# Kernel tuning notes

Measured on AMD Instinct MI355X. Metric: run time of the kernel, lower is better.

Reference implementation:

```python
import jax, jax.numpy as jnp
import numpy as np

N0, N1, N2 = 1200000, 120000, 12000  # nodes per hop (outermost -> seeds)
E0, E1 = 1200000, 120000
IN_C, HID_C, OUT_C = 256, 256, 64


def setup_inputs() -> dict:
    key = jax.random.key(0)
    ks = jax.random.split(key, 10)
    s_in, s_hid = 1.0 / np.sqrt(IN_C), 1.0 / np.sqrt(HID_C)
    return {
        "x": jax.random.normal(ks[0], (N0, IN_C), dtype=jnp.float32),
        "src0": jax.random.randint(ks[1], (E0,), 0, N0, dtype=jnp.int64),
        "dst0": jax.random.randint(ks[2], (E0,), 0, N1, dtype=jnp.int64),
        "src1": jax.random.randint(ks[3], (E1,), 0, N1, dtype=jnp.int64),
        "dst1": jax.random.randint(ks[4], (E1,), 0, N2, dtype=jnp.int64),
        "Wl0": jax.random.normal(ks[5], (HID_C, IN_C), dtype=jnp.float32) * s_in,
        "b0": jnp.zeros((HID_C,), dtype=jnp.float32),
        "Wr0": jax.random.normal(ks[6], (HID_C, IN_C), dtype=jnp.float32) * s_in,
        "Wl1": jax.random.normal(ks[7], (OUT_C, HID_C), dtype=jnp.float32) * s_hid,
        "b1": jnp.zeros((OUT_C,), dtype=jnp.float32),
        "Wr1": jax.random.normal(ks[8], (OUT_C, HID_C), dtype=jnp.float32) * s_hid,
    }


def _sage_conv(x_src, x_tgt, src, dst, Wl, b, Wr, n_tgt):
    # gather neighbor (source) features, mean-scatter onto targets
    msg = x_src[src]                                          # [E, C]
    agg = jax.ops.segment_sum(msg, dst, num_segments=n_tgt)   # [n_tgt, C]
    cnt = jax.ops.segment_sum(jnp.ones((dst.shape[0],), x_src.dtype), dst,
                              num_segments=n_tgt)
    agg = agg / jnp.maximum(cnt, 1.0)[:, None]
    return agg @ Wl.T + b + x_tgt @ Wr.T


def reference(x, src0, dst0, src1, dst1, Wl0, b0, Wr0, Wl1, b1, Wr1):
    # layer 0 (eval mode: dropout is identity)
    h = _sage_conv(x, x[:N1], src0, dst0, Wl0, b0, Wr0, N1)
    h = jax.nn.relu(h)
    # layer 1
    out = _sage_conv(h, h[:N2], src1, dst1, Wl1, b1, Wr1, N2)
    return jax.nn.log_softmax(out, axis=-1)
```

## Files before the change

kernel.cpp:

```cpp
#include <hip/hip_runtime.h>

#define N0c 1200000
#define N1c 120000
#define N2c 12000
#define E0c 1200000
#define E1c 120000
#define NB0 118
#define NB1 12

typedef short short8 __attribute__((ext_vector_type(8)));
typedef float f32x4 __attribute__((ext_vector_type(4)));
typedef unsigned short u16;

__device__ __forceinline__ u16 f2bf(float f) {
    union { float f; unsigned u; } v; v.f = f;
    unsigned r = v.u + 0x7FFFu + ((v.u >> 16) & 1u);
    return (u16)(r >> 16);
}
__device__ __forceinline__ float bf2f(u16 h) {
    union { unsigned u; float f; } v; v.u = ((unsigned)h) << 16;
    return v.f;
}

__global__ void k_hist(const int* __restrict__ dst0, const int* __restrict__ dst1,
                       int* __restrict__ c0, int* __restrict__ c1) {
    int i = blockIdx.x * 256 + threadIdx.x;
    int part = blockIdx.x & 7;
    if (i < E0c) atomicAdd(&c0[part * N1c + dst0[i]], 1);
    else if (i < E0c + E1c) atomicAdd(&c1[part * N2c + dst1[i - E0c]], 1);
}

__global__ void k_scanA(const int* __restrict__ c0, const int* __restrict__ c1,
                        int* __restrict__ partials) {
    __shared__ int sh[256];
    int hop = blockIdx.x >= NB0;
    int blk = hop ? blockIdx.x - NB0 : blockIdx.x;
    const int* c = hop ? c1 : c0;
    int n = hop ? N2c : N1c;
    int d0 = blk * 1024 + threadIdx.x * 4;
    int tsum = 0;
#pragma unroll
    for (int j = 0; j < 4; ++j) {
        int d = d0 + j;
        if (d < n)
#pragma unroll
            for (int k = 0; k < 8; ++k) tsum += c[k * n + d];
    }
    sh[threadIdx.x] = tsum;
    __syncthreads();
    for (int ofs = 128; ofs > 0; ofs >>= 1) {
        if (threadIdx.x < ofs) sh[threadIdx.x] += sh[threadIdx.x + ofs];
        __syncthreads();
    }
    if (threadIdx.x == 0) partials[blockIdx.x] = sh[0];
}

__global__ void k_scanB(int* __restrict__ partials, int* __restrict__ rs0,
                        int* __restrict__ rs1) {
    __shared__ int sh[256];
    int tid = threadIdx.x;
    int v0 = tid < NB0 ? partials[tid] : 0;
    sh[tid] = v0; __syncthreads();
    for (int ofs = 1; ofs < 256; ofs <<= 1) {
        int t = tid >= ofs ? sh[tid - ofs] : 0;
        __syncthreads();
        sh[tid] += t;
        __syncthreads();
    }
    if (tid < NB0) partials[tid] = sh[tid] - v0;
    __syncthreads();
    int v1 = tid < NB1 ? partials[NB0 + tid] : 0;
    sh[tid] = v1; __syncthreads();
    for (int ofs = 1; ofs < 256; ofs <<= 1) {
        int t = tid >= ofs ? sh[tid - ofs] : 0;
        __syncthreads();
        sh[tid] += t;
        __syncthreads();
    }
    if (tid < NB1) partials[NB0 + tid] = sh[tid] - v1;
    if (tid == 0) { rs0[N1c] = E0c; rs1[N2c] = E1c; }
}

__global__ void k_scanC(const int* __restrict__ c0, const int* __restrict__ c1,
                        const int* __restrict__ partials, int* __restrict__ rs0,
                        int* __restrict__ rs1, int* __restrict__ bs0,
                        int* __restrict__ bs1) {
    __shared__ int sh[256];
    int hop = blockIdx.x >= NB0;
    int blk = hop ? blockIdx.x - NB0 : blockIdx.x;
    const int* c = hop ? c1 : c0;
    int* rs = hop ? rs1 : rs0;
    int* bs = hop ? bs1 : bs0;
    int n = hop ? N2c : N1c;
    int tid = threadIdx.x;
    int d0 = blk * 1024 + tid * 4;
    int cv[4][8];
    int tsum = 0;
#pragma unroll
    for (int j = 0; j < 4; ++j)
#pragma unroll
        for (int k = 0; k < 8; ++k) {
            int d = d0 + j;
            int v = (d < n) ? c[k * n + d] : 0;
            cv[j][k] = v; tsum += v;
        }
    sh[tid] = tsum; __syncthreads();
    for (int ofs = 1; ofs < 256; ofs <<= 1) {
        int t = tid >= ofs ? sh[tid - ofs] : 0;
        __syncthreads();
        sh[tid] += t;
        __syncthreads();
    }
    int run = partials[blockIdx.x] + sh[tid] - tsum;
#pragma unroll
    for (int j = 0; j < 4; ++j) {
        int d = d0 + j;
        if (d < n) {
            rs[d] = run;
#pragma unroll
            for (int k = 0; k < 8; ++k) { bs[k * n + d] = run; run += cv[j][k]; }
        }
    }
}

__global__ void k_scat(const int* __restrict__ src0, const int* __restrict__ dst0,
                       const int* __restrict__ src1, const int* __restrict__ dst1,
                       int* __restrict__ c0, int* __restrict__ c1,
                       const int* __restrict__ bs0, const int* __restrict__ bs1,
                       int* __restrict__ eidx0, int* __restrict__ eidx1) {
    int i = blockIdx.x * 256 + threadIdx.x;
    int part = blockIdx.x & 7;
    if (i < E0c) {
        int d = dst0[i];
        int off = atomicSub(&c0[part * N1c + d], 1) - 1;
        eidx0[bs0[part * N1c + d] + off] = src0[i];
    } else if (i < E0c + E1c) {
        int j = i - E0c;
        int d = dst1[j];
        int off = atomicSub(&c1[part * N2c + d], 1) - 1;
        eidx1[bs1[part * N2c + d] + off] = src1[j];
    }
}

__global__ void k_wcat2(u16* __restrict__ Bt0, const float* __restrict__ Wl0,
                        const float* __restrict__ Wr0, u16* __restrict__ Bt1,
                        const float* __restrict__ Wl1, const float* __restrict__ Wr1) {
    int i = blockIdx.x * blockDim.x + threadIdx.x;
    if (i < 256 * 512) {
        int c = i >> 9, k = i & 511;
        float v = (k < 256) ? Wl0[c * 256 + k] : Wr0[c * 256 + (k - 256)];
        Bt0[i] = f2bf(v);
    } else if (i < 256 * 512 + 128 * 512) {
        int j = i - 256 * 512;
        int c = j >> 9, k = j & 511;
        float v = 0.f;
        if (c < 64) v = (k < 256) ? Wl1[c * 256 + k] : Wr1[c * 256 + (k - 256)];
        Bt1[j] = f2bf(v);
    }
}

__global__ void k_agg0(const float* __restrict__ x, const int* __restrict__ eidx,
                       const int* __restrict__ rs, u16* __restrict__ A, int ntgt) {
    int w = (int)((blockIdx.x * blockDim.x + threadIdx.x) >> 6);
    int lane = threadIdx.x & 63;
    if (w >= ntgt) return;
    int s = rs[w], e = rs[w + 1];
    float a0 = 0.f, a1 = 0.f, a2 = 0.f, a3 = 0.f;
    int i = s;
    for (; i + 8 <= e; i += 8) {
        float4 v[8];
#pragma unroll
        for (int u = 0; u < 8; ++u) {
            long idx = eidx[i + u];
            v[u] = ((const float4*)(x + idx * 256))[lane];
        }
#pragma unroll
        for (int u = 0; u < 8; ++u) {
            a0 += v[u].x; a1 += v[u].y; a2 += v[u].z; a3 += v[u].w;
        }
    }
    for (; i + 2 <= e; i += 2) {
        long i0 = eidx[i], i1 = eidx[i + 1];
        float4 v0 = ((const float4*)(x + i0 * 256))[lane];
        float4 v1 = ((const float4*)(x + i1 * 256))[lane];
        a0 += v0.x + v1.x; a1 += v0.y + v1.y; a2 += v0.z + v1.z; a3 += v0.w + v1.w;
    }
    if (i < e) {
        long idx = eidx[i];
        float4 v = ((const float4*)(x + idx * 256))[lane];
        a0 += v.x; a1 += v.y; a2 += v.z; a3 += v.w;
    }
    int c = e - s; if (c < 1) c = 1;
    float sc = 1.f / (float)c;
    ushort4 o;
    o.x = f2bf(a0 * sc); o.y = f2bf(a1 * sc); o.z = f2bf(a2 * sc); o.w = f2bf(a3 * sc);
    *(ushort4*)(A + (long)w * 512 + lane * 4) = o;
    float4 sv = ((const float4*)(x + (long)w * 256))[lane];
    ushort4 so;
    so.x = f2bf(sv.x); so.y = f2bf(sv.y); so.z = f2bf(sv.z); so.w = f2bf(sv.w);
    *(ushort4*)(A + (long)w * 512 + 256 + lane * 4) = so;
}

__global__ void k_agg1(const u16* __restrict__ hsrc, const int* __restrict__ eidx,
                       const int* __restrict__ rs, u16* __restrict__ A, int ntgt) {
    int w = (int)((blockIdx.x * blockDim.x + threadIdx.x) >> 6);
    int lane = threadIdx.x & 63;
    if (w >= ntgt) return;
    int s = rs[w], e = rs[w + 1];
    float a0 = 0.f, a1 = 0.f, a2 = 0.f, a3 = 0.f;
    int i = s;
    for (; i + 4 <= e; i += 4) {
        long i0 = eidx[i], i1 = eidx[i + 1], i2 = eidx[i + 2], i3 = eidx[i + 3];
        ushort4 v0 = ((const ushort4*)(hsrc + i0 * 256))[lane];
        ushort4 v1 = ((const ushort4*)(hsrc + i1 * 256))[lane];
        ushort4 v2 = ((const ushort4*)(hsrc + i2 * 256))[lane];
        ushort4 v3 = ((const ushort4*)(hsrc + i3 * 256))[lane];
        a0 += (bf2f(v0.x) + bf2f(v1.x)) + (bf2f(v2.x) + bf2f(v3.x));
        a1 += (bf2f(v0.y) + bf2f(v1.y)) + (bf2f(v2.y) + bf2f(v3.y));
        a2 += (bf2f(v0.z) + bf2f(v1.z)) + (bf2f(v2.z) + bf2f(v3.z));
        a3 += (bf2f(v0.w) + bf2f(v1.w)) + (bf2f(v2.w) + bf2f(v3.w));
    }
    for (; i < e; ++i) {
        long idx = eidx[i];
        ushort4 v = ((const ushort4*)(hsrc + idx * 256))[lane];
        a0 += bf2f(v.x); a1 += bf2f(v.y); a2 += bf2f(v.z); a3 += bf2f(v.w);
    }
    int c = e - s; if (c < 1) c = 1;
    float sc = 1.f / (float)c;
    ushort4 o;
    o.x = f2bf(a0 * sc); o.y = f2bf(a1 * sc); o.z = f2bf(a2 * sc); o.w = f2bf(a3 * sc);
    *(ushort4*)(A + (long)w * 512 + lane * 4) = o;
    ushort4 sv = ((const ushort4*)(hsrc + (long)w * 256))[lane];
    *(ushort4*)(A + (long)w * 512 + 256 + lane * 4) = sv;
}

#define BM 128
#define BK 32
#define LDK 40

template <int WN, bool RELU_BF16>
__global__ __launch_bounds__(128 * WN)
void k_gemm(const u16* __restrict__ A, const u16* __restrict__ Bt,
            const float* __restrict__ bias, void* __restrict__ outp,
            int M, int Ncols, int ldo) {
    constexpr int BN_ = WN * 64;
    constexpr int APT = 4 / WN;
    constexpr int WSH = (WN == 4) ? 2 : 1;
    __shared__ u16 As[BM * LDK];
    __shared__ u16 Bs[BN_ * LDK];
    const int tid = threadIdx.x;
    const int lane = tid & 63, wid = tid >> 6;
    const int wm = wid >> WSH, wn = wid & (WN - 1);
    const long m0 = (long)blockIdx.x * BM;
    const int n0 = blockIdx.y * BN_;
    const int sar = tid / WN, sac = (tid % WN) * (APT * 8);
    const int sbr = tid >> 1, sbc = (tid & 1) * 16;

    f32x4 acc[4][4];
#pragma unroll
    for (int i = 0; i < 4; ++i)
#pragma unroll
        for (int j = 0; j < 4; ++j) acc[i][j] = (f32x4){0.f, 0.f, 0.f, 0.f};

    int4 ra[APT]; int4 rb[2];

    auto load_tile = [&](int ks) {
        int k0 = ks * BK;
        const int4* p = (const int4*)(A + (m0 + sar) * 512 + k0 + sac);
#pragma unroll
        for (int t = 0; t < APT; ++t) ra[t] = p[t];
        const int4* q = (const int4*)(Bt + (long)(n0 + sbr) * 512 + k0 + sbc);
        rb[0] = q[0]; rb[1] = q[1];
    };

    auto write_tile = [&]() {
        int4* da = (int4*)(As + sar * LDK + sac);
#pragma unroll
        for (int t = 0; t < APT; ++t) da[t] = ra[t];
        int4* db = (int4*)(Bs + sbr * LDK + sbc);
        db[0] = rb[0]; db[1] = rb[1];
    };

    load_tile(0);
    const int NK = 512 / BK;
    for (int ks = 0; ks < NK; ++ks) {
        __syncthreads();
        write_tile();
        __syncthreads();
        if (ks + 1 < NK) load_tile(ks + 1);
        short8 af[4], bv[4];
        const int rr = lane & 15, gg = lane >> 4;
#pragma unroll
        for (int f = 0; f < 4; ++f) {
            af[f] = *(const short8*)(As + (wm * 64 + f * 16 + rr) * LDK + gg * 8);
            bv[f] = *(const short8*)(Bs + (wn * 64 + f * 16 + rr) * LDK + gg * 8);
        }
#pragma unroll
        for (int i = 0; i < 4; ++i)
#pragma unroll
            for (int j = 0; j < 4; ++j)
                acc[i][j] =
                    __builtin_amdgcn_mfma_f32_16x16x32_bf16(af[i], bv[j], acc[i][j], 0, 0, 0);
    }

#pragma unroll
    for (int j = 0; j < 4; ++j) {
        int col = n0 + wn * 64 + j * 16 + (lane & 15);
        if (col >= Ncols) continue;
        float bvl = bias[col];
#pragma unroll
        for (int i = 0; i < 4; ++i) {
            long row = m0 + wm * 64 + i * 16 + (lane >> 4) * 4;
#pragma unroll
            for (int q = 0; q < 4; ++q) {
                long r = row + q;
                if (r < M) {
                    float v = acc[i][j][q] + bvl;
                    if (RELU_BF16) {
                        v = v > 0.f ? v : 0.f;
                        ((u16*)outp)[r * (long)ldo + col] = f2bf(v);
                    } else {
                        ((float*)outp)[r * (long)ldo + col] = v;
                    }
                }
            }
        }
    }
}

__global__ void k_lsm(const float* __restrict__ lg, float* __restrict__ out, int nrows) {
    int w = (int)((blockIdx.x * blockDim.x + threadIdx.x) >> 6);
    int lane = threadIdx.x & 63;
    if (w >= nrows) return;
    float v = lg[(long)w * 64 + lane];
    float m = v;
    for (int d = 32; d > 0; d >>= 1) m = fmaxf(m, __shfl_xor(m, d, 64));
    float ex = __expf(v - m);
    float s = ex;
    for (int d = 32; d > 0; d >>= 1) s += __shfl_xor(s, d, 64);
    out[(long)w * 64 + lane] = v - m - __logf(s);
}

extern "C" void kernel_launch(void* const* d_in, const int* in_sizes, int n_in,
                              void* d_out, int out_size, void* d_ws, size_t ws_size,
                              hipStream_t stream) {
    const float* x   = (const float*)d_in[0];
    const int* src0  = (const int*)d_in[1];
    const int* dst0  = (const int*)d_in[2];
    const int* src1  = (const int*)d_in[3];
    const int* dst1  = (const int*)d_in[4];
    const float* Wl0 = (const float*)d_in[5];
    const float* b0  = (const float*)d_in[6];
    const float* Wr0 = (const float*)d_in[7];
    const float* Wl1 = (const float*)d_in[8];
    const float* b1  = (const float*)d_in[9];
    const float* Wr1 = (const float*)d_in[10];

    char* base = (char*)d_ws;
    size_t off = 0;
    auto alloc = [&](size_t bytes) -> void* {
        off = (off + 255) & ~(size_t)255;
        void* p = base + off;
        off += bytes;
        return p;
    };
    const int N1pad = 120064, N2pad = 12032;
    int* c0       = (int*)alloc((size_t)8 * N1c * 4);
    int* c1       = (int*)alloc((size_t)8 * N2c * 4);
    int* bs0      = (int*)alloc((size_t)8 * N1c * 4);
    int* bs1      = (int*)alloc((size_t)8 * N2c * 4);
    int* rs0      = (int*)alloc((size_t)(N1c + 1) * 4);
    int* rs1      = (int*)alloc((size_t)(N2c + 1) * 4);
    int* partials = (int*)alloc((size_t)(NB0 + NB1) * 4);
    int* eidx0    = (int*)alloc((size_t)E0c * 4);
    int* eidx1    = (int*)alloc((size_t)E1c * 4);
    u16* A0       = (u16*)alloc((size_t)N1pad * 512 * 2);
    u16* hbuf     = (u16*)alloc((size_t)N1pad * 256 * 2);
    u16* A1       = (u16*)alloc((size_t)N2pad * 512 * 2);
    u16* Bt0      = (u16*)alloc((size_t)256 * 512 * 2);
    u16* Bt1      = (u16*)alloc((size_t)128 * 512 * 2);
    float* logits = (float*)alloc((size_t)N2pad * 64 * 4);

    hipMemsetAsync(c0, 0, (size_t)8 * (N1c + N2c) * 4, stream);

    const int Etot = E0c + E1c;
    k_hist<<<(Etot + 255) / 256, 256, 0, stream>>>(dst0, dst1, c0, c1);
    k_scanA<<<NB0 + NB1, 256, 0, stream>>>(c0, c1, partials);
    k_scanB<<<1, 256, 0, stream>>>(partials, rs0, rs1);
    k_scanC<<<NB0 + NB1, 256, 0, stream>>>(c0, c1, partials, rs0, rs1, bs0, bs1);
    k_scat<<<(Etot + 255) / 256, 256, 0, stream>>>(src0, dst0, src1, dst1,
                                                   c0, c1, bs0, bs1, eidx0, eidx1);

    k_wcat2<<<(256 * 512 + 128 * 512 + 255) / 256, 256, 0, stream>>>(Bt0, Wl0, Wr0,
                                                                     Bt1, Wl1, Wr1);

    k_agg0<<<(N1c + 3) / 4, 256, 0, stream>>>(x, eidx0, rs0, A0, N1c);
    dim3 g0(N1pad / BM, 1);
    k_gemm<4, true><<<g0, 512, 0, stream>>>(A0, Bt0, b0, hbuf, N1c, 256, 256);

    k_agg1<<<(N2c + 3) / 4, 256, 0, stream>>>(hbuf, eidx1, rs1, A1, N2c);
    dim3 g1(N2pad / BM, 1);
    k_gemm<2, false><<<g1, 256, 0, stream>>>(A1, Bt1, b1, logits, N2c, 64, 64);

    k_lsm<<<(N2c + 3) / 4, 256, 0, stream>>>(logits, (float*)d_out, N2c);
}
```

Before: 592.0 us.

## Fuse neighbor aggregation into GEMM via swizzled LDS A-tile, fold log-softmax

Each layer's mean aggregation now writes its bf16 concatenated [agg | self] row block straight into a 128KB XOR-swizzled shared-memory tile, and the block then runs the MFMA GEMM from that tile. This removes the global A0/A1 round trips and separate kernel launches. Layer 1 also computes log-softmax in the GEMM epilogue with 16-lane shuffles, which drops the logits buffer and the k_lsm kernel. In exchange, 128KB of LDS per block limits occupancy to about one block per CU, so the latency-bound gather phase gets less parallelism and cannot overlap with the GEMM.

```diff
diff --git a/kernel.cpp b/kernel.cpp
--- a/kernel.cpp
+++ b/kernel.cpp
@@ -150,150 +150,98 @@
         int c = i >> 9, k = i & 511;
         float v = (k < 256) ? Wl0[c * 256 + k] : Wr0[c * 256 + (k - 256)];
         Bt0[i] = f2bf(v);
-    } else if (i < 256 * 512 + 128 * 512) {
+    } else if (i < 256 * 512 + 64 * 512) {
         int j = i - 256 * 512;
         int c = j >> 9, k = j & 511;
-        float v = 0.f;
-        if (c < 64) v = (k < 256) ? Wl1[c * 256 + k] : Wr1[c * 256 + (k - 256)];
+        float v = (k < 256) ? Wl1[c * 256 + k] : Wr1[c * 256 + (k - 256)];
         Bt1[j] = f2bf(v);
     }
 }
 
-__global__ void k_agg0(const float* __restrict__ x, const int* __restrict__ eidx,
-                       const int* __restrict__ rs, u16* __restrict__ A, int ntgt) {
-    int w = (int)((blockIdx.x * blockDim.x + threadIdx.x) >> 6);
-    int lane = threadIdx.x & 63;
-    if (w >= ntgt) return;
-    int s = rs[w], e = rs[w + 1];
-    float a0 = 0.f, a1 = 0.f, a2 = 0.f, a3 = 0.f;
-    int i = s;
-    for (; i + 8 <= e; i += 8) {
-        float4 v[8];
-#pragma unroll
-        for (int u = 0; u < 8; ++u) {
-            long idx = eidx[i + u];
-            v[u] = ((const float4*)(x + idx * 256))[lane];
-        }
-#pragma unroll
-        for (int u = 0; u < 8; ++u) {
-            a0 += v[u].x; a1 += v[u].y; a2 += v[u].z; a3 += v[u].w;
-        }
-    }
-    for (; i + 2 <= e; i += 2) {
-        long i0 = eidx[i], i1 = eidx[i + 1];
-        float4 v0 = ((const float4*)(x + i0 * 256))[lane];
-        float4 v1 = ((const float4*)(x + i1 * 256))[lane];
-        a0 += v0.x + v1.x; a1 += v0.y + v1.y; a2 += v0.z + v1.z; a3 += v0.w + v1.w;
-    }
-    if (i < e) {
-        long idx = eidx[i];
-        float4 v = ((const float4*)(x + idx * 256))[lane];
-        a0 += v.x; a1 += v.y; a2 += v.z; a3 += v.w;
-    }
-    int c = e - s; if (c < 1) c = 1;
-    float sc = 1.f / (float)c;
-    ushort4 o;
-    o.x = f2bf(a0 * sc); o.y = f2bf(a1 * sc); o.z = f2bf(a2 * sc); o.w = f2bf(a3 * sc);
-    *(ushort4*)(A + (long)w * 512 + lane * 4) = o;
-    float4 sv = ((const float4*)(x + (long)w * 256))[lane];
-    ushort4 so;
-    so.x = f2bf(sv.x); so.y = f2bf(sv.y); so.z = f2bf(sv.z); so.w = f2bf(sv.w);
-    *(ushort4*)(A + (long)w * 512 + 256 + lane * 4) = so;
-}
-
-__global__ void k_agg1(const u16* __restrict__ hsrc, const int* __restrict__ eidx,
-                       const int* __restrict__ rs, u16* __restrict__ A, int ntgt) {
-    int w = (int)((blockIdx.x * blockDim.x + threadIdx.x) >> 6);
-    int lane = threadIdx.x & 63;
-    if (w >= ntgt) return;
-    int s = rs[w], e = rs[w + 1];
-    float a0 = 0.f, a1 = 0.f, a2 = 0.f, a3 = 0.f;
-    int i = s;
-    for (; i + 4 <= e; i += 4) {
-        long i0 = eidx[i], i1 = eidx[i + 1], i2 = eidx[i + 2], i3 = eidx[i + 3];
-        ushort4 v0 = ((const ushort4*)(hsrc + i0 * 256))[lane];
-        ushort4 v1 = ((const ushort4*)(hsrc + i1 * 256))[lane];
-        ushort4 v2 = ((const ushort4*)(hsrc + i2 * 256))[lane];
-        ushort4 v3 = ((const ushort4*)(hsrc + i3 * 256))[lane];
-        a0 += (bf2f(v0.x) + bf2f(v1.x)) + (bf2f(v2.x) + bf2f(v3.x));
-        a1 += (bf2f(v0.y) + bf2f(v1.y)) + (bf2f(v2.y) + bf2f(v3.y));
-        a2 += (bf2f(v0.z) + bf2f(v1.z)) + (bf2f(v2.z) + bf2f(v3.z));
-        a3 += (bf2f(v0.w) + bf2f(v1.w)) + (bf2f(v2.w) + bf2f(v3.w));
-    }
-    for (; i < e; ++i) {
-        long idx = eidx[i];
-        ushort4 v = ((const ushort4*)(hsrc + idx * 256))[lane];
-        a0 += bf2f(v.x); a1 += bf2f(v.y); a2 += bf2f(v.z); a3 += bf2f(v.w);
-    }
-    int c = e - s; if (c < 1) c = 1;
-    float sc = 1.f / (float)c;
-    ushort4 o;
-    o.x = f2bf(a0 * sc); o.y = f2bf(a1 * sc); o.z = f2bf(a2 * sc); o.w = f2bf(a3 * sc);
-    *(ushort4*)(A + (long)w * 512 + lane * 4) = o;
-    ushort4 sv = ((const ushort4*)(hsrc + (long)w * 256))[lane];
-    *(ushort4*)(A + (long)w * 512 + 256 + lane * 4) = sv;
-}
-
-#define BM 128
-#define BK 32
-#define LDK 40
-
-template <int WN, bool RELU_BF16>
-__global__ __launch_bounds__(128 * WN)
-void k_gemm(const u16* __restrict__ A, const u16* __restrict__ Bt,
-            const float* __restrict__ bias, void* __restrict__ outp,
-            int M, int Ncols, int ldo) {
-    constexpr int BN_ = WN * 64;
-    constexpr int APT = 4 / WN;
-    constexpr int WSH = (WN == 4) ? 2 : 1;
-    __shared__ u16 As[BM * LDK];
-    __shared__ u16 Bs[BN_ * LDK];
+__device__ __forceinline__ int aoff(int row, int byteInRow) {
+    return row * 1024 + (byteInRow ^ ((row & 7) << 4));
+}
+
+__global__ __launch_bounds__(512)
+void k_fused0(const float* __restrict__ x, const int* __restrict__ eidx,
+              const int* __restrict__ rs, const u16* __restrict__ Bt,
+              const float* __restrict__ bias, u16* __restrict__ outp) {
+    __shared__ u16 Asm[128 * 512];
+    __shared__ u16 Bsm[256 * 40];
     const int tid = threadIdx.x;
     const int lane = tid & 63, wid = tid >> 6;
-    const int wm = wid >> WSH, wn = wid & (WN - 1);
-    const long m0 = (long)blockIdx.x * BM;
-    const int n0 = blockIdx.y * BN_;
-    const int sar = tid / WN, sac = (tid % WN) * (APT * 8);
-    const int sbr = tid >> 1, sbc = (tid & 1) * 16;
-
+    const long m0 = (long)blockIdx.x * 128;
+
+    for (int t = 0; t < 16; ++t) {
+        int wl = wid * 16 + t;
+        long w = m0 + wl;
+        float a0 = 0.f, a1 = 0.f, a2 = 0.f, a3 = 0.f;
+        float s0 = 0.f, s1 = 0.f, s2 = 0.f, s3 = 0.f;
+        if (w < N1c) {
+            int s = rs[w], e = rs[w + 1];
+            int i = s;
+            for (; i + 8 <= e; i += 8) {
+                float4 v[8];
+#pragma unroll
+                for (int u = 0; u < 8; ++u)
+                    v[u] = ((const float4*)(x + (long)eidx[i + u] * 256))[lane];
+#pragma unroll
+                for (int u = 0; u < 8; ++u) {
+                    a0 += v[u].x; a1 += v[u].y; a2 += v[u].z; a3 += v[u].w;
+                }
+            }
+            for (; i + 2 <= e; i += 2) {
+                float4 v0 = ((const float4*)(x + (long)eidx[i] * 256))[lane];
+                float4 v1 = ((const float4*)(x + (long)eidx[i + 1] * 256))[lane];
+                a0 += v0.x + v1.x; a1 += v0.y + v1.y;
+                a2 += v0.z + v1.z; a3 += v0.w + v1.w;
+            }
+            if (i < e) {
+                float4 v = ((const float4*)(x + (long)eidx[i] * 256))[lane];
+                a0 += v.x; a1 += v.y; a2 += v.z; a3 += v.w;
+            }
+            int c = e - s; if (c < 1) c = 1;
+            float sc = 1.f / (float)c;
+            a0 *= sc; a1 *= sc; a2 *= sc; a3 *= sc;
+            float4 sv = ((const float4*)(x + w * 256))[lane];
+            s0 = sv.x; s1 = sv.y; s2 = sv.z; s3 = sv.w;
+        }
+        ushort4 oa; oa.x = f2bf(a0); oa.y = f2bf(a1); oa.z = f2bf(a2); oa.w = f2bf(a3);
+        *(ushort4*)((char*)Asm + aoff(wl, lane * 8)) = oa;
+        ushort4 os; os.x = f2bf(s0); os.y = f2bf(s1); os.z = f2bf(s2); os.w = f2bf(s3);
+        *(ushort4*)((char*)Asm + aoff(wl, 512 + lane * 8)) = os;
+    }
+
+    const int wm = wid >> 2, wn = wid & 3;
+    const int brow = tid >> 1, bcol = (tid & 1) * 16;
     f32x4 acc[4][4];
 #pragma unroll
     for (int i = 0; i < 4; ++i)
 #pragma unroll
         for (int j = 0; j < 4; ++j) acc[i][j] = (f32x4){0.f, 0.f, 0.f, 0.f};
-
-    int4 ra[APT]; int4 rb[2];
-
-    auto load_tile = [&](int ks) {
-        int k0 = ks * BK;
-        const int4* p = (const int4*)(A + (m0 + sar) * 512 + k0 + sac);
-#pragma unroll
-        for (int t = 0; t < APT; ++t) ra[t] = p[t];
-        const int4* q = (const int4*)(Bt + (long)(n0 + sbr) * 512 + k0 + sbc);
-        rb[0] = q[0]; rb[1] = q[1];
-    };
-
-    auto write_tile = [&]() {
-        int4* da = (int4*)(As + sar * LDK + sac);
-#pragma unroll
-        for (int t = 0; t < APT; ++t) da[t] = ra[t];
-        int4* db = (int4*)(Bs + sbr * LDK + sbc);
-        db[0] = rb[0]; db[1] = rb[1];
-    };
-
-    load_tile(0);
-    const int NK = 512 / BK;
-    for (int ks = 0; ks < NK; ++ks) {
-        __syncthreads();
-        write_tile();
-        __syncthreads();
-        if (ks + 1 < NK) load_tile(ks + 1);
+    int4 rb0, rb1;
+    {
+        const int4* q = (const int4*)(Bt + (long)brow * 512 + bcol);
+        rb0 = q[0]; rb1 = q[1];
+    }
+    __syncthreads();
+    const int rr = lane & 15, gg = lane >> 4;
+    for (int ks = 0; ks < 16; ++ks) {
+        {
+            int4* d = (int4*)(Bsm + brow * 40 + bcol);
+            d[0] = rb0; d[1] = rb1;
+        }
+        __syncthreads();
+        if (ks < 15) {
+            const int4* q = (const int4*)(Bt + (long)brow * 512 + (ks + 1) * 32 + bcol);
+            rb0 = q[0]; rb1 = q[1];
+        }
         short8 af[4], bv[4];
-        const int rr = lane & 15, gg = lane >> 4;
 #pragma unroll
         for (int f = 0; f < 4; ++f) {
-            af[f] = *(const short8*)(As + (wm * 64 + f * 16 + rr) * LDK + gg * 8);
-            bv[f] = *(const short8*)(Bs + (wn * 64 + f * 16 + rr) * LDK + gg * 8);
+            af[f] = *(const short8*)((char*)Asm +
+                                     aoff(wm * 64 + f * 16 + rr, ks * 64 + gg * 16));
+            bv[f] = *(const short8*)(Bsm + (wn * 64 + f * 16 + rr) * 40 + gg * 8);
         }
 #pragma unroll
         for (int i = 0; i < 4; ++i)
@@ -301,44 +249,135 @@
             for (int j = 0; j < 4; ++j)
                 acc[i][j] =
                     __builtin_amdgcn_mfma_f32_16x16x32_bf16(af[i], bv[j], acc[i][j], 0, 0, 0);
+        __syncthreads();
     }
 
 #pragma unroll
     for (int j = 0; j < 4; ++j) {
-        int col = n0 + wn * 64 + j * 16 + (lane & 15);
-        if (col >= Ncols) continue;
+        int col = wn * 64 + j * 16 + rr;
         float bvl = bias[col];
 #pragma unroll
         for (int i = 0; i < 4; ++i) {
-            long row = m0 + wm * 64 + i * 16 + (lane >> 4) * 4;
+            long row = m0 + wm * 64 + i * 16 + gg * 4;
 #pragma unroll
             for (int q = 0; q < 4; ++q) {
                 long r = row + q;
-                if (r < M) {
+                if (r < N1c) {
                     float v = acc[i][j][q] + bvl;
-                    if (RELU_BF16) {
-                        v = v > 0.f ? v : 0.f;
-                        ((u16*)outp)[r * (long)ldo + col] = f2bf(v);
-                    } else {
-                        ((float*)outp)[r * (long)ldo + col] = v;
-                    }
+                    v = v > 0.f ? v : 0.f;
+                    outp[r * 256 + col] = f2bf(v);
                 }
             }
         }
     }
 }
 
-__global__ void k_lsm(const float* __restrict__ lg, float* __restrict__ out, int nrows) {
-    int w = (int)((blockIdx.x * blockDim.x + threadIdx.x) >> 6);
-    int lane = threadIdx.x & 63;
-    if (w >= nrows) return;
-    float v = lg[(long)w * 64 + lane];
-    float m = v;
-    for (int d = 32; d > 0; d >>= 1) m = fmaxf(m, __shfl_xor(m, d, 64));
-    float ex = __expf(v - m);
-    float s = ex;
-    for (int d = 32; d > 0; d >>= 1) s += __shfl_xor(s, d, 64);
-    out[(long)w * 64 + lane] = v - m - __logf(s);
+__global__ __launch_bounds__(256)
+void k_fused1(const u16* __restrict__ hsrc, const int* __restrict__ eidx,
+              const int* __restrict__ rs, const u16* __restrict__ Bt,
+              const float* __restrict__ bias, float* __restrict__ outp) {
+    __shared__ u16 Asm[128 * 512];
+    __shared__ u16 Bsm[64 * 40];
+    const int tid = threadIdx.x;
+    const int lane = tid & 63, wid = tid >> 6;
+    const long m0 = (long)blockIdx.x * 128;
+
+    for (int t = 0; t < 32; ++t) {
+        int wl = wid * 32 + t;
+        long w = m0 + wl;
+        float a0 = 0.f, a1 = 0.f, a2 = 0.f, a3 = 0.f;
+        ushort4 sv; sv.x = 0; sv.y = 0; sv.z = 0; sv.w = 0;
+        if (w < N2c) {
+            int s = rs[w], e = rs[w + 1];
+            int i = s;
+            for (; i + 4 <= e; i += 4) {
+                ushort4 v0 = ((const ushort4*)(hsrc + (long)eidx[i] * 256))[lane];
+                ushort4 v1 = ((const ushort4*)(hsrc + (long)eidx[i + 1] * 256))[lane];
+                ushort4 v2 = ((const ushort4*)(hsrc + (long)eidx[i + 2] * 256))[lane];
+                ushort4 v3 = ((const ushort4*)(hsrc + (long)eidx[i + 3] * 256))[lane];
+                a0 += (bf2f(v0.x) + bf2f(v1.x)) + (bf2f(v2.x) + bf2f(v3.x));
+                a1 += (bf2f(v0.y) + bf2f(v1.y)) + (bf2f(v2.y) + bf2f(v3.y));
+                a2 += (bf2f(v0.z) + bf2f(v1.z)) + (bf2f(v2.z) + bf2f(v3.z));
+                a3 += (bf2f(v0.w) + bf2f(v1.w)) + (bf2f(v2.w) + bf2f(v3.w));
+            }
+            for (; i < e; ++i) {
+                ushort4 v = ((const ushort4*)(hsrc + (long)eidx[i] * 256))[lane];
+                a0 += bf2f(v.x); a1 += bf2f(v.y); a2 += bf2f(v.z); a3 += bf2f(v.w);
+            }
+            int c = e - s; if (c < 1) c = 1;
+            float sc = 1.f / (float)c;
+            a0 *= sc; a1 *= sc; a2 *= sc; a3 *= sc;
+            sv = ((const ushort4*)(hsrc + w * 256))[lane];
+        }
+        ushort4 oa; oa.x = f2bf(a0); oa.y = f2bf(a1); oa.z = f2bf(a2); oa.w = f2bf(a3);
+        *(ushort4*)((char*)Asm + aoff(wl, lane * 8)) = oa;
+        *(ushort4*)((char*)Asm + aoff(wl, 512 + lane * 8)) = sv;
+    }
+
+    const int wm = wid;
+    const bool bact = tid < 128;
+    const int brow = tid >> 1, bcol = (tid & 1) * 16;
+    f32x4 acc[2][4];
+#pragma unroll
+    for (int i = 0; i < 2; ++i)
+#pragma unroll
+        for (int j = 0; j < 4; ++j) acc[i][j] = (f32x4){0.f, 0.f, 0.f, 0.f};
+    int4 rb0, rb1;
+    if (bact) {
+        const int4* q = (const int4*)(Bt + (long)brow * 512 + bcol);
+        rb0 = q[0]; rb1 = q[1];
+    }
+    __syncthreads();
+    const int rr = lane & 15, gg = lane >> 4;
+    for (int ks = 0; ks < 16; ++ks) {
+        if (bact) {
+            int4* d = (int4*)(Bsm + brow * 40 + bcol);
+            d[0] = rb0; d[1] = rb1;
+        }
+        __syncthreads();
+        if (bact && ks < 15) {
+            const int4* q = (const int4*)(Bt + (long)brow * 512 + (ks + 1) * 32 + bcol);
+            rb0 = q[0]; rb1 = q[1];
+        }
+        short8 af[2], bv[4];
+#pragma unroll
+        for (int f = 0; f < 2; ++f)
+            af[f] = *(const short8*)((char*)Asm +
+                                     aoff(wm * 32 + f * 16 + rr, ks * 64 + gg * 16));
+#pragma unroll
+        for (int j = 0; j < 4; ++j)
+            bv[j] = *(const short8*)(Bsm + (j * 16 + rr) * 40 + gg * 8);
+#pragma unroll
+        for (int i = 0; i < 2; ++i)
+#pragma unroll
+            for (int j = 0; j < 4; ++j)
+                acc[i][j] =
+                    __builtin_amdgcn_mfma_f32_16x16x32_bf16(af[i], bv[j], acc[i][j], 0, 0, 0);
+        __syncthreads();
+    }
+
+#pragma unroll
+    for (int i = 0; i < 2; ++i) {
+#pragma unroll
+        for (int q = 0; q < 4; ++q) {
+            long r = m0 + wm * 32 + i * 16 + gg * 4 + q;
+            float v[4];
+#pragma unroll
+            for (int j = 0; j < 4; ++j) v[j] = acc[i][j][q] + bias[j * 16 + rr];
+            float mx = fmaxf(fmaxf(v[0], v[1]), fmaxf(v[2], v[3]));
+#pragma unroll
+            for (int msk = 1; msk < 16; msk <<= 1) mx = fmaxf(mx, __shfl_xor(mx, msk, 16));
+            float se = __expf(v[0] - mx) + __expf(v[1] - mx) +
+                       __expf(v[2] - mx) + __expf(v[3] - mx);
+#pragma unroll
+            for (int msk = 1; msk < 16; msk <<= 1) se += __shfl_xor(se, msk, 16);
+            float ln = __logf(se);
+            if (r < N2c) {
+#pragma unroll
+                for (int j = 0; j < 4; ++j) outp[r * 64 + j * 16 + rr] = v[j] - mx - ln;
+            }
+        }
+    }
 }
 
 extern "C" void kernel_launch(void* const* d_in, const int* in_sizes, int n_in,
@@ -364,7 +403,6 @@
         off += bytes;
         return p;
     };
-    const int N1pad = 120064, N2pad = 12032;
     int* c0       = (int*)alloc((size_t)8 * N1c * 4);
     int* c1       = (int*)alloc((size_t)8 * N2c * 4);
     int* bs0      = (int*)alloc((size_t)8 * N1c * 4);
@@ -374,12 +412,9 @@
     int* partials = (int*)alloc((size_t)(NB0 + NB1) * 4);
     int* eidx0    = (int*)alloc((size_t)E0c * 4);
     int* eidx1    = (int*)alloc((size_t)E1c * 4);
-    u16* A0       = (u16*)alloc((size_t)N1pad * 512 * 2);
-    u16* hbuf     = (u16*)alloc((size_t)N1pad * 256 * 2);
-    u16* A1       = (u16*)alloc((size_t)N2pad * 512 * 2);
+    u16* hbuf     = (u16*)alloc((size_t)N1c * 256 * 2);
     u16* Bt0      = (u16*)alloc((size_t)256 * 512 * 2);
-    u16* Bt1      = (u16*)alloc((size_t)128 * 512 * 2);
-    float* logits = (float*)alloc((size_t)N2pad * 64 * 4);
+    u16* Bt1      = (u16*)alloc((size_t)64 * 512 * 2);
 
     hipMemsetAsync(c0, 0, (size_t)8 * (N1c + N2c) * 4, stream);
 
@@ -391,16 +426,11 @@
     k_scat<<<(Etot + 255) / 256, 256, 0, stream>>>(src0, dst0, src1, dst1,
                                                    c0, c1, bs0, bs1, eidx0, eidx1);
 
-    k_wcat2<<<(256 * 512 + 128 * 512 + 255) / 256, 256, 0, stream>>>(Bt0, Wl0, Wr0,
-                                                                     Bt1, Wl1, Wr1);
-
-    k_agg0<<<(N1c + 3) / 4, 256, 0, stream>>>(x, eidx0, rs0, A0, N1c);
-    dim3 g0(N1pad / BM, 1);
-    k_gemm<4, true><<<g0, 512, 0, stream>>>(A0, Bt0, b0, hbuf, N1c, 256, 256);
-
-    k_agg1<<<(N2c + 3) / 4, 256, 0, stream>>>(hbuf, eidx1, rs1, A1, N2c);
-    dim3 g1(N2pad / BM, 1);
-    k_gemm<2, false><<<g1, 256, 0, stream>>>(A1, Bt1, b1, logits, N2c, 64, 64);
-
-    k_lsm<<<(N2c + 3) / 4, 256, 0, stream>>>(logits, (float*)d_out, N2c);
-}
+    k_wcat2<<<(256 * 512 + 64 * 512 + 255) / 256, 256, 0, stream>>>(Bt0, Wl0, Wr0,
+                                                                    Bt1, Wl1, Wr1);
+
+    k_fused0<<<(N1c + 127) / 128, 512, 0, stream>>>(x, eidx0, rs0, Bt0, b0, hbuf);
+
+    k_fused1<<<(N2c + 127) / 128, 256, 0, stream>>>(hbuf, eidx1, rs1, Bt1, b1,
+                                                    (float*)d_out);
+}
```

After: 652.8 us. 10.3% more time.

## Pre-tile A0 and Bt0 into padded k-slabs and add an async-LDS-load layer-0 GEMM

Applied to the files above, without the earlier changes.

The layer-0 activation matrix and weights are now stored as k-tiled slabs of 32 bf16 values padded to 40 per row, so each 128-row tile is one contiguous chunk. A new dedicated GEMM kernel copies those chunks straight into LDS with global_load_lds, double-buffered, and runs 16x16x32 bf16 MFMAs with a fused bias and ReLU epilogue. The aim is cheaper, bank-conflict-free tile staging and overlap of loads with compute. The cost is a scattered write pattern in the aggregation kernel and an epilogue that writes scalar, poorly coalesced bf16 values.

```diff
diff --git a/kernel.cpp b/kernel.cpp
--- a/kernel.cpp
+++ b/kernel.cpp
@@ -1,4 +1,5 @@
 #include <hip/hip_runtime.h>
+#include <stdint.h>
 
 #define N0c 1200000
 #define N1c 120000
@@ -7,6 +8,10 @@
 #define E1c 120000
 #define NB0 118
 #define NB1 12
+#define N1pad 120064
+#define N2pad 12032
+#define ROWB 80
+#define ROWU 40
 
 typedef short short8 __attribute__((ext_vector_type(8)));
 typedef float f32x4 __attribute__((ext_vector_type(4)));
@@ -20,6 +25,12 @@
 __device__ __forceinline__ float bf2f(u16 h) {
     union { unsigned u; float f; } v; v.u = ((unsigned)h) << 16;
     return v.f;
+}
+
+__device__ __forceinline__ void gload16(const char* g, char* l) {
+    __builtin_amdgcn_global_load_lds(
+        (const __attribute__((address_space(1))) void*)g,
+        (__attribute__((address_space(3))) void*)l, 16, 0, 0);
 }
 
 __global__ void k_hist(const int* __restrict__ dst0, const int* __restrict__ dst1,
@@ -149,7 +160,7 @@
     if (i < 256 * 512) {
         int c = i >> 9, k = i & 511;
         float v = (k < 256) ? Wl0[c * 256 + k] : Wr0[c * 256 + (k - 256)];
-        Bt0[i] = f2bf(v);
+        Bt0[((size_t)(k >> 5) * 256 + c) * ROWU + (k & 31)] = f2bf(v);
     } else if (i < 256 * 512 + 128 * 512) {
         int j = i - 256 * 512;
         int c = j >> 9, k = j & 511;
@@ -170,35 +181,33 @@
     for (; i + 8 <= e; i += 8) {
         float4 v[8];
 #pragma unroll
-        for (int u = 0; u < 8; ++u) {
-            long idx = eidx[i + u];
-            v[u] = ((const float4*)(x + idx * 256))[lane];
-        }
+        for (int u = 0; u < 8; ++u)
+            v[u] = ((const float4*)(x + (long)eidx[i + u] * 256))[lane];
 #pragma unroll
         for (int u = 0; u < 8; ++u) {
             a0 += v[u].x; a1 += v[u].y; a2 += v[u].z; a3 += v[u].w;
         }
     }
     for (; i + 2 <= e; i += 2) {
-        long i0 = eidx[i], i1 = eidx[i + 1];
-        float4 v0 = ((const float4*)(x + i0 * 256))[lane];
-        float4 v1 = ((const float4*)(x + i1 * 256))[lane];
+        float4 v0 = ((const float4*)(x + (long)eidx[i] * 256))[lane];
+        float4 v1 = ((const float4*)(x + (long)eidx[i + 1] * 256))[lane];
         a0 += v0.x + v1.x; a1 += v0.y + v1.y; a2 += v0.z + v1.z; a3 += v0.w + v1.w;
     }
     if (i < e) {
-        long idx = eidx[i];
-        float4 v = ((const float4*)(x + idx * 256))[lane];
+        float4 v = ((const float4*)(x + (long)eidx[i] * 256))[lane];
         a0 += v.x; a1 += v.y; a2 += v.z; a3 += v.w;
     }
     int c = e - s; if (c < 1) c = 1;
     float sc = 1.f / (float)c;
-    ushort4 o;
-    o.x = f2bf(a0 * sc); o.y = f2bf(a1 * sc); o.z = f2bf(a2 * sc); o.w = f2bf(a3 * sc);
-    *(ushort4*)(A + (long)w * 512 + lane * 4) = o;
+    int kt = lane >> 3;
+    int cu = (lane & 7) * 4;
+    ushort4 oa;
+    oa.x = f2bf(a0 * sc); oa.y = f2bf(a1 * sc); oa.z = f2bf(a2 * sc); oa.w = f2bf(a3 * sc);
+    *(ushort4*)(A + ((size_t)kt * N1pad + w) * ROWU + cu) = oa;
     float4 sv = ((const float4*)(x + (long)w * 256))[lane];
-    ushort4 so;
-    so.x = f2bf(sv.x); so.y = f2bf(sv.y); so.z = f2bf(sv.z); so.w = f2bf(sv.w);
-    *(ushort4*)(A + (long)w * 512 + 256 + lane * 4) = so;
+    ushort4 os;
+    os.x = f2bf(sv.x); os.y = f2bf(sv.y); os.z = f2bf(sv.z); os.w = f2bf(sv.w);
+    *(ushort4*)(A + ((size_t)(kt + 8) * N1pad + w) * ROWU + cu) = os;
 }
 
 __global__ void k_agg1(const u16* __restrict__ hsrc, const int* __restrict__ eidx,
@@ -210,19 +219,17 @@
     float a0 = 0.f, a1 = 0.f, a2 = 0.f, a3 = 0.f;
     int i = s;
     for (; i + 4 <= e; i += 4) {
-        long i0 = eidx[i], i1 = eidx[i + 1], i2 = eidx[i + 2], i3 = eidx[i + 3];
-        ushort4 v0 = ((const ushort4*)(hsrc + i0 * 256))[lane];
-        ushort4 v1 = ((const ushort4*)(hsrc + i1 * 256))[lane];
-        ushort4 v2 = ((const ushort4*)(hsrc + i2 * 256))[lane];
-        ushort4 v3 = ((const ushort4*)(hsrc + i3 * 256))[lane];
+        ushort4 v0 = ((const ushort4*)(hsrc + (long)eidx[i] * 256))[lane];
+        ushort4 v1 = ((const ushort4*)(hsrc + (long)eidx[i + 1] * 256))[lane];
+        ushort4 v2 = ((const ushort4*)(hsrc + (long)eidx[i + 2] * 256))[lane];
+        ushort4 v3 = ((const ushort4*)(hsrc + (long)eidx[i + 3] * 256))[lane];
         a0 += (bf2f(v0.x) + bf2f(v1.x)) + (bf2f(v2.x) + bf2f(v3.x));
         a1 += (bf2f(v0.y) + bf2f(v1.y)) + (bf2f(v2.y) + bf2f(v3.y));
         a2 += (bf2f(v0.z) + bf2f(v1.z)) + (bf2f(v2.z) + bf2f(v3.z));
         a3 += (bf2f(v0.w) + bf2f(v1.w)) + (bf2f(v2.w) + bf2f(v3.w));
     }
     for (; i < e; ++i) {
-        long idx = eidx[i];
-        ushort4 v = ((const ushort4*)(hsrc + idx * 256))[lane];
+        ushort4 v = ((const ushort4*)(hsrc + (long)eidx[i] * 256))[lane];
         a0 += bf2f(v.x); a1 += bf2f(v.y); a2 += bf2f(v.z); a3 += bf2f(v.w);
     }
     int c = e - s; if (c < 1) c = 1;
@@ -232,6 +239,80 @@
     *(ushort4*)(A + (long)w * 512 + lane * 4) = o;
     ushort4 sv = ((const ushort4*)(hsrc + (long)w * 256))[lane];
     *(ushort4*)(A + (long)w * 512 + 256 + lane * 4) = sv;
+}
+
+__global__ __launch_bounds__(512)
+void k_gemm0(const u16* __restrict__ A0, const u16* __restrict__ Bt,
+             const float* __restrict__ bias, u16* __restrict__ outp) {
+    __shared__ int4 Lbuf[2 * 30720 / 16];
+    char* L = (char*)Lbuf;
+    const int tid = threadIdx.x;
+    const int lane = tid & 63, wid = tid >> 6;
+    const int wm = wid >> 2, wn = wid & 3;
+    const long m0 = (long)blockIdx.x * 128;
+
+    f32x4 acc[4][4];
+#pragma unroll
+    for (int i = 0; i < 4; ++i)
+#pragma unroll
+        for (int j = 0; j < 4; ++j) acc[i][j] = (f32x4){0.f, 0.f, 0.f, 0.f};
+
+    const char* Abase = (const char*)A0 + m0 * ROWB;
+    const char* Bbase = (const char*)Bt;
+
+    auto stage = [&](int buf, int kt) {
+        char* lb = L + buf * 30720;
+        const char* ga = Abase + (size_t)kt * ((size_t)N1pad * ROWB);
+        const char* gb = Bbase + (size_t)kt * (256 * ROWB);
+#pragma unroll
+        for (int c0 = 0; c0 < 4; ++c0) {
+            int c = wid + c0 * 8;
+            if (c < 30) {
+                const char* g = (c < 10) ? (ga + c * 1024) : (gb + (c - 10) * 1024);
+                gload16(g + lane * 16, lb + c * 1024);
+            }
+        }
+    };
+
+    stage(0, 0);
+    const int rr = lane & 15, gg = lane >> 4;
+    for (int ks = 0; ks < 16; ++ks) {
+        int cur = ks & 1;
+        __syncthreads();
+        if (ks + 1 < 16) stage(cur ^ 1, ks + 1);
+        const char* lb = L + cur * 30720;
+        short8 af[4], bv[4];
+#pragma unroll
+        for (int f = 0; f < 4; ++f) {
+            af[f] = *(const short8*)(lb + (wm * 64 + f * 16 + rr) * ROWB + gg * 16);
+            bv[f] = *(const short8*)(lb + 10240 + (wn * 64 + f * 16 + rr) * ROWB + gg * 16);
+        }
+#pragma unroll
+        for (int i = 0; i < 4; ++i)
+#pragma unroll
+            for (int j = 0; j < 4; ++j)
+                acc[i][j] =
+                    __builtin_amdgcn_mfma_f32_16x16x32_bf16(af[i], bv[j], acc[i][j], 0, 0, 0);
+    }
+
+#pragma unroll
+    for (int j = 0; j < 4; ++j) {
+        int col = wn * 64 + j * 16 + rr;
+        float bvl = bias[col];
+#pragma unroll
+        for (int i = 0; i < 4; ++i) {
+            long row = m0 + wm * 64 + i * 16 + gg * 4;
+#pragma unroll
+            for (int q = 0; q < 4; ++q) {
+                long r = row + q;
+                if (r < N1c) {
+                    float v = acc[i][j][q] + bvl;
+                    v = v > 0.f ? v : 0.f;
+                    outp[r * 256 + col] = f2bf(v);
+                }
+            }
+        }
+    }
 }
 
 #define BM 128
@@ -364,7 +445,6 @@
         off += bytes;
         return p;
     };
-    const int N1pad = 120064, N2pad = 12032;
     int* c0       = (int*)alloc((size_t)8 * N1c * 4);
     int* c1       = (int*)alloc((size_t)8 * N2c * 4);
     int* bs0      = (int*)alloc((size_t)8 * N1c * 4);
@@ -374,10 +454,10 @@
     int* partials = (int*)alloc((size_t)(NB0 + NB1) * 4);
     int* eidx0    = (int*)alloc((size_t)E0c * 4);
     int* eidx1    = (int*)alloc((size_t)E1c * 4);
-    u16* A0       = (u16*)alloc((size_t)N1pad * 512 * 2);
+    u16* A0       = (u16*)alloc((size_t)16 * N1pad * ROWU * 2);
     u16* hbuf     = (u16*)alloc((size_t)N1pad * 256 * 2);
     u16* A1       = (u16*)alloc((size_t)N2pad * 512 * 2);
-    u16* Bt0      = (u16*)alloc((size_t)256 * 512 * 2);
+    u16* Bt0      = (u16*)alloc((size_t)16 * 256 * ROWU * 2);
     u16* Bt1      = (u16*)alloc((size_t)128 * 512 * 2);
     float* logits = (float*)alloc((size_t)N2pad * 64 * 4);
 
@@ -395,8 +475,7 @@
                                                                      Bt1, Wl1, Wr1);
 
     k_agg0<<<(N1c + 3) / 4, 256, 0, stream>>>(x, eidx0, rs0, A0, N1c);
-    dim3 g0(N1pad / BM, 1);
-    k_gemm<4, true><<<g0, 512, 0, stream>>>(A0, Bt0, b0, hbuf, N1c, 256, 256);
+    k_gemm0<<<N1pad / 128, 512, 0, stream>>>(A0, Bt0, b0, hbuf);
 
     k_agg1<<<(N2c + 3) / 4, 256, 0, stream>>>(hbuf, eidx1, rs1, A1, N2c);
     dim3 g1(N2pad / BM, 1);
```

Result: no change. 584.7 us (-1.2%).
